# Kernel optimization log

Measured on AMD Instinct MI355X. Metric: run time of the kernel, lower is better.

## Reference

```python
import jax, jax.numpy as jnp
import numpy as np

B, L, D_MODEL = 4, 2048, 1024
D_INNER, D_STATE, D_CONV = 2 * D_MODEL, 16, 4
DT_RANK = (D_MODEL + 15) // 16  # 64


def silu(v):
    return v * jax.nn.sigmoid(v)


def setup_inputs() -> dict:
    key = jax.random.key(0)
    ks = jax.random.split(key, 8)
    n = lambda k, shape, s: jax.random.normal(k, shape, jnp.float32) * s
    A = jnp.broadcast_to(jnp.arange(1, D_STATE + 1, dtype=jnp.float32), (D_INNER, D_STATE))
    return {
        "x": jax.random.normal(ks[0], (B, L, D_MODEL), jnp.float32),
        "in_proj_w": n(ks[1], (2 * D_INNER, D_MODEL), 0.02),
        "conv_w": n(ks[2], (D_INNER, 1, D_CONV), 0.1),
        "conv_b": jnp.zeros((D_INNER,), jnp.float32),
        "x_proj_w": n(ks[3], (DT_RANK + 2 * D_STATE, D_INNER), 0.02),
        "dt_proj_w": n(ks[4], (D_INNER, DT_RANK), 0.1),
        "dt_proj_b": n(ks[5], (D_INNER,), 0.1),
        "A_log": jnp.log(A),
        "D": jnp.ones((D_INNER,), jnp.float32),
        "out_proj_w": n(ks[6], (D_MODEL, D_INNER), 0.02),
        "ln_g": jnp.ones((D_MODEL,), jnp.float32),
        "ln_b": jnp.zeros((D_MODEL,), jnp.float32),
    }


def mamba(x, in_proj_w, conv_w, conv_b, x_proj_w, dt_proj_w, dt_proj_b, A_log, D, out_proj_w):
    # in_proj -> (B, L, 2*d_inner), split into x-branch and gate z
    xz = jnp.einsum("bld,ed->ble", x, in_proj_w)
    xm, z = jnp.split(xz, 2, axis=-1)
    # depthwise causal conv over time
    xc = jnp.swapaxes(xm, 1, 2)  # (B, d_inner, L)
    xc = jax.lax.conv_general_dilated(
        xc, conv_w, (1,), [(D_CONV - 1, 0)],
        dimension_numbers=("NCH", "OIH", "NCH"), feature_group_count=D_INNER,
    ) + conv_b[None, :, None]
    xm = silu(jnp.swapaxes(xc, 1, 2))  # (B, L, d_inner)
    # input-dependent dt, B, C
    dbc = jnp.einsum("bld,ed->ble", xm, x_proj_w)
    dt, Bm, Cm = jnp.split(dbc, [DT_RANK, DT_RANK + D_STATE], axis=-1)
    dt = jax.nn.softplus(jnp.einsum("blr,dr->bld", dt, dt_proj_w) + dt_proj_b)
    A = -jnp.exp(A_log)  # (d_inner, d_state)

    def step(h, inp):
        dt_t, B_t, C_t, x_t = inp  # (B,d_inner),(B,d_state),(B,d_state),(B,d_inner)
        h = jnp.exp(dt_t[..., None] * A) * h + (dt_t * x_t)[..., None] * B_t[:, None, :]
        y = jnp.einsum("bds,bs->bd", h, C_t)
        return h, y

    h0 = jnp.zeros((B, D_INNER, D_STATE), xm.dtype)
    xs = (jnp.swapaxes(dt, 0, 1), jnp.swapaxes(Bm, 0, 1), jnp.swapaxes(Cm, 0, 1), jnp.swapaxes(xm, 0, 1))
    _, ys = jax.lax.scan(step, h0, xs)
    y = jnp.swapaxes(ys, 0, 1) + D * xm  # (B, L, d_inner)
    y = y * silu(z)
    return jnp.einsum("bld,od->blo", y, out_proj_w)


def layer_norm(h, g, b, eps=1e-5):
    mu = jnp.mean(h, axis=-1, keepdims=True)
    var = jnp.mean(jnp.square(h - mu), axis=-1, keepdims=True)
    return (h - mu) * jax.lax.rsqrt(var + eps) * g + b


def reference(x, in_proj_w, conv_w, conv_b, x_proj_w, dt_proj_w, dt_proj_b, A_log, D, out_proj_w, ln_g, ln_b):
    y = mamba(x, in_proj_w, conv_w, conv_b, x_proj_w, dt_proj_w, dt_proj_b, A_log, D, out_proj_w)
    # dropout_level=0 (eval): identity
    return layer_norm(y + x, ln_g, ln_b)
```

## Files before the change

### kernel.cpp

```cpp
#include <hip/hip_runtime.h>
#include <hip/hip_bf16.h>

#define B_ 4
#define L_ 2048
#define DM 1024
#define DI 2048
#define DSTATE 16
#define DTR 64
#define LC 64
#define NC (L_ / LC)
#define LOG2E 1.44269504f

typedef unsigned short ushort_t;
typedef __bf16 bf16x8 __attribute__((ext_vector_type(8)));
typedef float f32x4 __attribute__((ext_vector_type(4)));
typedef float f32x16 __attribute__((ext_vector_type(16)));
typedef unsigned short u16x8 __attribute__((ext_vector_type(8)));
typedef unsigned short u16x4 __attribute__((ext_vector_type(4)));

__device__ __forceinline__ ushort_t f2bf(float f) {
    unsigned u = __builtin_bit_cast(unsigned, f);
    unsigned r = (u + 0x7FFFu + ((u >> 16) & 1u)) >> 16;
    return (ushort_t)r;
}
__device__ __forceinline__ float bf2f(ushort_t h) {
    unsigned u = ((unsigned)h) << 16;
    return __builtin_bit_cast(float, u);
}

#define CV_E0 1048576
#define CV_E1 (CV_E0 + 49152)
#define CV_E2 (CV_E1 + 32768)
#define CV_E3 (CV_E2 + 524288)
#define CV_E4 (CV_E3 + 2097152)
__global__ __launch_bounds__(256) void k_cvt5(
    const float* __restrict__ s0, ushort_t* __restrict__ d0,
    const float* __restrict__ s1, ushort_t* __restrict__ d1,
    const float* __restrict__ s2, ushort_t* __restrict__ d2,
    const float* __restrict__ s3, ushort_t* __restrict__ d3,
    const float* __restrict__ s4, ushort_t* __restrict__ d4) {
    int g = blockIdx.x * 256 + threadIdx.x;
    const float* s;
    ushort_t* dst;
    int i;
    if (g < CV_E0)      { s = s0; dst = d0; i = g * 4; }
    else if (g < CV_E1) { s = s1; dst = d1; i = (g - CV_E0) * 4; }
    else if (g < CV_E2) { s = s2; dst = d2; i = (g - CV_E1) * 4; }
    else if (g < CV_E3) { s = s3; dst = d3; i = (g - CV_E2) * 4; }
    else                { s = s4; dst = d4; i = (g - CV_E3) * 4; }
    float4 v = *reinterpret_cast<const float4*>(s + i);
    ushort4 o;
    o.x = f2bf(v.x); o.y = f2bf(v.y); o.z = f2bf(v.z); o.w = f2bf(v.w);
    *reinterpret_cast<ushort4*>(dst + i) = o;
}

#define FENCE asm volatile("" ::: "memory")
#define VM3 asm volatile("s_waitcnt vmcnt(3)" ::: "memory")
#define VM0 asm volatile("s_waitcnt vmcnt(0)" ::: "memory")

template <int KK, int LDC, int NT>
__global__ __launch_bounds__(512, 2) void k_gemmP(const ushort_t* __restrict__ Aq,
                                                  const ushort_t* __restrict__ Bq,
                                                  ushort_t* __restrict__ C) {
    __shared__ ushort_t lds[36864];
    const int tid = threadIdx.x;
    const int w = tid >> 6, lane = tid & 63;
    const int l15 = lane & 15;
    const int wm = w >> 2, wn = w & 3;
    const int bid = blockIdx.x;
    const int tm = bid & 31, tn = bid >> 5;
    const int row0 = tm * 256, col0 = tn * 128;

    const int rs = w * 16 + (lane >> 2);
    const int lcs = (lane & 3) ^ ((lane >> 3) & 3);
    const int pcr = ((lane >> 4) ^ ((l15 >> 1) & 3)) * 8;
    const int aoff = wm * 4096 + l15 * 32 + pcr;
    const int boff = 8192 + wn * 1024 + l15 * 32 + pcr;

    auto stg = [&](int buf, int t) {
        const ushort_t* sa = Aq + (size_t)(row0 + rs) * KK + t * 32 + lcs * 8;
        __builtin_amdgcn_global_load_lds(
            (const __attribute__((address_space(1))) void*)sa,
            (__attribute__((address_space(3))) void*)&lds[buf * 12288 + w * 512], 16, 0, 0);
        __builtin_amdgcn_global_load_lds(
            (const __attribute__((address_space(1))) void*)(sa + (size_t)128 * KK),
            (__attribute__((address_space(3))) void*)&lds[buf * 12288 + 4096 + w * 512], 16, 0, 0);
        const ushort_t* sb = Bq + (size_t)(col0 + rs) * KK + t * 32 + lcs * 8;
        __builtin_amdgcn_global_load_lds(
            (const __attribute__((address_space(1))) void*)sb,
            (__attribute__((address_space(3))) void*)&lds[buf * 12288 + 8192 + w * 512], 16, 0, 0);
    };

    f32x4 acc[8][2] = {};

#define GPHASE(BUF, STAGE_STMT, WAIT_STMT)                                        \
    {                                                                             \
        bf16x8 av[8], bv[2];                                                      \
        _Pragma("unroll") for (int i_ = 0; i_ < 8; ++i_)                          \
            av[i_] = *(const bf16x8*)&lds[(BUF) * 12288 + aoff + i_ * 512];       \
        _Pragma("unroll") for (int i_ = 0; i_ < 2; ++i_)                          \
            bv[i_] = *(const bf16x8*)&lds[(BUF) * 12288 + boff + i_ * 512];       \
        STAGE_STMT;                                                               \
        FENCE; __builtin_amdgcn_s_barrier(); FENCE;                               \
        asm volatile("s_waitcnt lgkmcnt(0)" ::: "memory");                        \
        __builtin_amdgcn_sched_barrier(0);                                        \
        __builtin_amdgcn_s_setprio(1);                                            \
        _Pragma("unroll") for (int i_ = 0; i_ < 8; ++i_)                          \
            _Pragma("unroll") for (int j_ = 0; j_ < 2; ++j_)                      \
                acc[i_][j_] = __builtin_amdgcn_mfma_f32_16x16x32_bf16(            \
                    av[i_], bv[j_], acc[i_][j_], 0, 0, 0);                        \
        __builtin_amdgcn_s_setprio(0);                                            \
        WAIT_STMT;                                                                \
        FENCE; __builtin_amdgcn_s_barrier(); FENCE;                               \
    }

    stg(0, 0); stg(1, 1);
    VM3;
    FENCE; __builtin_amdgcn_s_barrier(); FENCE;

#pragma unroll 1
    for (int k = 0; k < (NT - 2) / 3; ++k) {
        const int t0 = 3 * k;
        GPHASE(0, stg(2, t0 + 2), VM3);
        GPHASE(1, stg(0, t0 + 3), VM3);
        GPHASE(2, stg(1, t0 + 4), VM3);
    }
    if constexpr ((NT - 2) % 3 == 2) {
        GPHASE(0, stg(2, NT - 2), VM3);
        GPHASE(1, stg(0, NT - 1), VM3);
        GPHASE(2, (void)0, VM0);
        GPHASE(0, (void)0, (void)0);
    } else {
        GPHASE(0, (void)0, VM0);
        GPHASE(1, (void)0, (void)0);
    }
#undef GPHASE

#pragma unroll
    for (int mf = 0; mf < 8; ++mf)
#pragma unroll
        for (int nf = 0; nf < 2; ++nf) {
            int col = col0 + wn * 32 + nf * 16 + l15;
#pragma unroll
            for (int r = 0; r < 4; ++r) {
                int row = row0 + wm * 128 + mf * 16 + (lane >> 4) * 4 + r;
                C[(size_t)row * LDC + col] = f2bf(acc[mf][nf][r]);
            }
        }
}

template <int EPI, bool OUTBF>
__global__ __launch_bounds__(256) void k_gemm2(
    const ushort_t* __restrict__ A, const ushort_t* __restrict__ Bw,
    void* __restrict__ C, const float* __restrict__ bias,
    int M, int N, int K, int lda, int ldb, int ldc, int tilesM) {
    __shared__ ushort_t As[128 * 64];
    __shared__ ushort_t Bs[128 * 64];
    int tid = threadIdx.x;
    int lane = tid & 63, wv = tid >> 6;
    int wr = wv >> 1, wc = wv & 1;
    int bid = blockIdx.x;
    int tilesN = gridDim.x / tilesM;
    int per = 8 * tilesN;
    int grp = bid / per, within = bid % per;
    int tm = grp * 8 + (within & 7);
    int tn = within >> 3;
    int row0 = tm * 128, col0 = tn * 128;
    int kchunk = K / gridDim.z;
    int kbeg = blockIdx.z * kchunk, kend = kbeg + kchunk;
    float* Cf = (float*)C + (size_t)blockIdx.z * (size_t)M * ldc;

    int sr = lane >> 3;
    int sj = lane & 7;
    f32x4 acc[4][4] = {};

    for (int k0 = kbeg; k0 < kend; k0 += 64) {
        __syncthreads();
#pragma unroll
        for (int i = 0; i < 4; ++i) {
            int slot = wv * 4 + i;
            int r = slot * 8 + sr;
            int jA = sj ^ (r & 7);
            __builtin_amdgcn_global_load_lds(
                (const __attribute__((address_space(1))) void*)&A[(size_t)(row0 + r) * lda + k0 + jA * 8],
                (__attribute__((address_space(3))) void*)&As[slot * 512], 16, 0, 0);
            __builtin_amdgcn_global_load_lds(
                (const __attribute__((address_space(1))) void*)&Bw[(size_t)(col0 + r) * ldb + k0 + jA * 8],
                (__attribute__((address_space(3))) void*)&Bs[slot * 512], 16, 0, 0);
        }
        __syncthreads();
#pragma unroll
        for (int kk = 0; kk < 2; ++kk) {
            int co = kk * 32 + (lane >> 4) * 8;
            int sx = (lane & 7) << 3;
            bf16x8 af[4], bfr[4];
#pragma unroll
            for (int m = 0; m < 4; ++m) {
                int rw = wr * 64 + m * 16 + (lane & 15);
                af[m] = *reinterpret_cast<const bf16x8*>(&As[rw * 64 + (co ^ sx)]);
            }
#pragma unroll
            for (int n = 0; n < 4; ++n) {
                int rw = wc * 64 + n * 16 + (lane & 15);
                bfr[n] = *reinterpret_cast<const bf16x8*>(&Bs[rw * 64 + (co ^ sx)]);
            }
#pragma unroll
            for (int m = 0; m < 4; ++m)
#pragma unroll
                for (int n = 0; n < 4; ++n)
                    acc[m][n] = __builtin_amdgcn_mfma_f32_16x16x32_bf16(af[m], bfr[n], acc[m][n], 0, 0, 0);
        }
    }

#pragma unroll
    for (int m = 0; m < 4; ++m) {
#pragma unroll
        for (int n = 0; n < 4; ++n) {
            int col = col0 + wc * 64 + n * 16 + (lane & 15);
            if (col >= N) continue;
#pragma unroll
            for (int r = 0; r < 4; ++r) {
                int row = row0 + wr * 64 + m * 16 + (lane >> 4) * 4 + r;
                float v = acc[m][n][r];
                if (EPI == 1) {
                    v += bias[col];
                    v = (v > 20.f) ? v : log1pf(__expf(v));
                }
                if (OUTBF)
                    ((ushort_t*)C)[(size_t)row * ldc + col] = f2bf(v);
                else
                    Cf[(size_t)row * ldc + col] = v;
            }
        }
    }
}

__global__ __launch_bounds__(256) void k_red4(const float* __restrict__ p,
                                              ushort_t* __restrict__ o,
                                              int n, int stride) {
    int i = (blockIdx.x * 256 + threadIdx.x) * 4;
    if (i >= n) return;
    f32x4 a = *reinterpret_cast<const f32x4*>(&p[i]);
    f32x4 b = *reinterpret_cast<const f32x4*>(&p[i + stride]);
    f32x4 c = *reinterpret_cast<const f32x4*>(&p[i + 2 * stride]);
    f32x4 d = *reinterpret_cast<const f32x4*>(&p[i + 3 * stride]);
    ushort4 r;
    r.x = f2bf(a[0] + b[0] + c[0] + d[0]);
    r.y = f2bf(a[1] + b[1] + c[1] + d[1]);
    r.z = f2bf(a[2] + b[2] + c[2] + d[2]);
    r.w = f2bf(a[3] + b[3] + c[3] + d[3]);
    *reinterpret_cast<ushort4*>(&o[i]) = r;
}

__global__ __launch_bounds__(256) void k_conv(const ushort_t* __restrict__ xz,
                                              const float* __restrict__ w,
                                              const float* __restrict__ bias,
                                              ushort_t* __restrict__ out) {
    int d = blockIdx.x * 256 + threadIdx.x;
    int b = blockIdx.z;
    int t0 = blockIdx.y * 128;
    float w0 = w[d * 4 + 0], w1 = w[d * 4 + 1], w2 = w[d * 4 + 2], w3 = w[d * 4 + 3];
    float bi = bias[d];
    size_t base = ((size_t)b * L_) * (2 * DI) + d;
    size_t obase = ((size_t)b * L_) * DI + d;
    float x0 = (t0 >= 3) ? bf2f(xz[base + (size_t)(t0 - 3) * (2 * DI)]) : 0.f;
    float x1 = (t0 >= 2) ? bf2f(xz[base + (size_t)(t0 - 2) * (2 * DI)]) : 0.f;
    float x2 = (t0 >= 1) ? bf2f(xz[base + (size_t)(t0 - 1) * (2 * DI)]) : 0.f;
    for (int t = t0; t < t0 + 128; ++t) {
        float cur = bf2f(xz[base + (size_t)t * (2 * DI)]);
        float v = w0 * x0 + w1 * x1 + w2 * x2 + w3 * cur + bi;
        v = v / (1.f + __expf(-v));
        out[obase + (size_t)t * DI] = f2bf(v);
        x0 = x1; x1 = x2; x2 = cur;
    }
}

__global__ __launch_bounds__(256) void k_scan1(
    const ushort_t* __restrict__ dt, const ushort_t* __restrict__ xm,
    const ushort_t* __restrict__ dbc, const float* __restrict__ A_log,
    float* __restrict__ hfin, float* __restrict__ dtsum) {
    __shared__ float Bsh[LC][DSTATE];
    int tid = threadIdx.x;
    int d = blockIdx.x * 256 + tid;
    int c = blockIdx.y, b = blockIdx.z;
    f32x16 arow;
    float a1 = __expf(A_log[d * DSTATE]);
    bool ok = true;
#pragma unroll
    for (int s = 0; s < DSTATE; ++s) {
        float av = __expf(A_log[d * DSTATE + s]);
        arow[s] = -av * LOG2E;
        ok = ok && (fabsf(av - (float)(s + 1) * a1) <= 1e-4f * (float)(s + 1) * fabsf(a1) + 1e-6f);
    }
    float arow0 = -a1 * LOG2E;
    size_t rbase = (size_t)b * L_ + (size_t)c * LC;
    {
        int i = tid * 4;
        int t = i >> 4, s0 = i & 15;
        u16x4 v = *reinterpret_cast<const u16x4*>(&dbc[(rbase + t) * 96 + DTR + s0]);
#pragma unroll
        for (int j = 0; j < 4; ++j) Bsh[t][s0 + j] = bf2f(v[j]);
    }
    __syncthreads();
    f32x4 h0 = {}, h1 = {}, h2 = {}, h3 = {};
    float sd = 0.f;
    if (ok) {
        for (int t = 0; t < LC; ++t) {
            size_t ro = rbase + t;
            float dtv = bf2f(dt[ro * DI + d]);
            float xv = bf2f(xm[ro * DI + d]);
            float dx = dtv * xv;
            sd += dtv;
            float p = __builtin_amdgcn_exp2f(dtv * arow0);
            float p2 = p * p, p3 = p2 * p, p4 = p2 * p2;
            f32x4 ea = {p, p2, p3, p4};
            f32x4 eb = ea * p4, ec = eb * p4, ed = ec * p4;
            const f32x4* Bq = reinterpret_cast<const f32x4*>(&Bsh[t][0]);
            h0 = h0 * ea + Bq[0] * dx;
            h1 = h1 * eb + Bq[1] * dx;
            h2 = h2 * ec + Bq[2] * dx;
            h3 = h3 * ed + Bq[3] * dx;
        }
    } else {
        for (int t = 0; t < LC; ++t) {
            size_t ro = rbase + t;
            float dtv = bf2f(dt[ro * DI + d]);
            float xv = bf2f(xm[ro * DI + d]);
            float dx = dtv * xv;
            sd += dtv;
            const f32x4* Bq = reinterpret_cast<const f32x4*>(&Bsh[t][0]);
            f32x4 e0, e1, e2, e3;
#pragma unroll
            for (int j = 0; j < 4; ++j) {
                e0[j] = __builtin_amdgcn_exp2f(dtv * arow[j]);
                e1[j] = __builtin_amdgcn_exp2f(dtv * arow[4 + j]);
                e2[j] = __builtin_amdgcn_exp2f(dtv * arow[8 + j]);
                e3[j] = __builtin_amdgcn_exp2f(dtv * arow[12 + j]);
            }
            h0 = h0 * e0 + Bq[0] * dx;
            h1 = h1 * e1 + Bq[1] * dx;
            h2 = h2 * e2 + Bq[2] * dx;
            h3 = h3 * e3 + Bq[3] * dx;
        }
    }
    size_t hbase = (((size_t)b * NC + c) * DI + d) * DSTATE;
    *reinterpret_cast<f32x4*>(&hfin[hbase + 0]) = h0;
    *reinterpret_cast<f32x4*>(&hfin[hbase + 4]) = h1;
    *reinterpret_cast<f32x4*>(&hfin[hbase + 8]) = h2;
    *reinterpret_cast<f32x4*>(&hfin[hbase + 12]) = h3;
    dtsum[((size_t)b * NC + c) * DI + d] = sd;
}

__global__ __launch_bounds__(256) void k_scan2(
    float* __restrict__ hfin, const float* __restrict__ dtsum,
    const float* __restrict__ A_log) {
    int gid = blockIdx.x * 256 + threadIdx.x;
    int s = gid & (DSTATE - 1);
    int d = (gid >> 4) & (DI - 1);
    int b = gid >> 15;
    float Av = -__expf(A_log[d * DSTATE + s]) * LOG2E;
    float carry = 0.f;
    for (int c = 0; c < NC; ++c) {
        size_t idx = (((size_t)b * NC + c) * DI + d) * DSTATE + s;
        float loc = hfin[idx];
        hfin[idx] = carry;
        float sd = dtsum[((size_t)b * NC + c) * DI + d];
        carry = __builtin_amdgcn_exp2f(Av * sd) * carry + loc;
    }
}

__global__ __launch_bounds__(256) void k_scan3(
    const ushort_t* __restrict__ dt, const ushort_t* __restrict__ xm,
    const ushort_t* __restrict__ xz, const ushort_t* __restrict__ dbc,
    const float* __restrict__ A_log, const float* __restrict__ Dp,
    const float* __restrict__ hinit, ushort_t* __restrict__ yg) {
    __shared__ float Bsh[LC][DSTATE];
    __shared__ float Csh[LC][DSTATE];
    int tid = threadIdx.x;
    int d = blockIdx.x * 256 + tid;
    int c = blockIdx.y, b = blockIdx.z;
    f32x16 arow;
    float a1 = __expf(A_log[d * DSTATE]);
    bool ok = true;
#pragma unroll
    for (int s = 0; s < DSTATE; ++s) {
        float av = __expf(A_log[d * DSTATE + s]);
        arow[s] = -av * LOG2E;
        ok = ok && (fabsf(av - (float)(s + 1) * a1) <= 1e-4f * (float)(s + 1) * fabsf(a1) + 1e-6f);
    }
    float arow0 = -a1 * LOG2E;
    float Dd = Dp[d];
    size_t rbase = (size_t)b * L_ + (size_t)c * LC;
    {
        int e0 = tid * 8;
        int t = e0 >> 5, s0 = e0 & 31;
        u16x8 v = *reinterpret_cast<const u16x8*>(&dbc[(rbase + t) * 96 + DTR + s0]);
#pragma unroll
        for (int j = 0; j < 8; ++j) {
            int s = s0 + j;
            float f = bf2f(v[j]);
            if (s < DSTATE) Bsh[t][s] = f;
            else Csh[t][s - DSTATE] = f;
        }
    }
    __syncthreads();
    size_t hbase = (((size_t)b * NC + c) * DI + d) * DSTATE;
    f32x4 h0 = *reinterpret_cast<const f32x4*>(&hinit[hbase + 0]);
    f32x4 h1 = *reinterpret_cast<const f32x4*>(&hinit[hbase + 4]);
    f32x4 h2 = *reinterpret_cast<const f32x4*>(&hinit[hbase + 8]);
    f32x4 h3 = *reinterpret_cast<const f32x4*>(&hinit[hbase + 12]);
    if (ok) {
        for (int t = 0; t < LC; ++t) {
            size_t ro = rbase + t;
            float dtv = bf2f(dt[ro * DI + d]);
            float xv = bf2f(xm[ro * DI + d]);
            float zv = bf2f(xz[ro * (2 * DI) + DI + d]);
            float dx = dtv * xv;
            float p = __builtin_amdgcn_exp2f(dtv * arow0);
            float p2 = p * p, p3 = p2 * p, p4 = p2 * p2;
            f32x4 ea = {p, p2, p3, p4};
            f32x4 eb = ea * p4, ec = eb * p4, ed = ec * p4;
            const f32x4* Bq = reinterpret_cast<const f32x4*>(&Bsh[t][0]);
            const f32x4* Cq = reinterpret_cast<const f32x4*>(&Csh[t][0]);
            h0 = h0 * ea + Bq[0] * dx;
            h1 = h1 * eb + Bq[1] * dx;
            h2 = h2 * ec + Bq[2] * dx;
            h3 = h3 * ed + Bq[3] * dx;
            f32x4 y4 = h0 * Cq[0] + h1 * Cq[1] + h2 * Cq[2] + h3 * Cq[3];
            float y = (y4[0] + y4[1]) + (y4[2] + y4[3]) + Dd * xv;
            y *= zv / (1.f + __expf(-zv));
            yg[ro * DI + d] = f2bf(y);
        }
    } else {
        for (int t = 0; t < LC; ++t) {
            size_t ro = rbase + t;
            float dtv = bf2f(dt[ro * DI + d]);
            float xv = bf2f(xm[ro * DI + d]);
            float zv = bf2f(xz[ro * (2 * DI) + DI + d]);
            float dx = dtv * xv;
            const f32x4* Bq = reinterpret_cast<const f32x4*>(&Bsh[t][0]);
            const f32x4* Cq = reinterpret_cast<const f32x4*>(&Csh[t][0]);
            f32x4 e0, e1, e2, e3;
#pragma unroll
            for (int j = 0; j < 4; ++j) {
                e0[j] = __builtin_amdgcn_exp2f(dtv * arow[j]);
                e1[j] = __builtin_amdgcn_exp2f(dtv * arow[4 + j]);
                e2[j] = __builtin_amdgcn_exp2f(dtv * arow[8 + j]);
                e3[j] = __builtin_amdgcn_exp2f(dtv * arow[12 + j]);
            }
            h0 = h0 * e0 + Bq[0] * dx;
            h1 = h1 * e1 + Bq[1] * dx;
            h2 = h2 * e2 + Bq[2] * dx;
            h3 = h3 * e3 + Bq[3] * dx;
            f32x4 y4 = h0 * Cq[0] + h1 * Cq[1] + h2 * Cq[2] + h3 * Cq[3];
            float y = (y4[0] + y4[1]) + (y4[2] + y4[3]) + Dd * xv;
            y *= zv / (1.f + __expf(-zv));
            yg[ro * DI + d] = f2bf(y);
        }
    }
}

__global__ __launch_bounds__(256) void k_ln(const ushort_t* __restrict__ mo,
                                            const float* __restrict__ x,
                                            const float* __restrict__ g,
                                            const float* __restrict__ be,
                                            float* __restrict__ out) {
    __shared__ float red[8];
    size_t r = blockIdx.x;
    int tid = threadIdx.x;
    ushort4 mv = *reinterpret_cast<const ushort4*>(&mo[r * DM + tid * 4]);
    float4 xv = *reinterpret_cast<const float4*>(&x[r * DM + tid * 4]);
    float h0 = bf2f(mv.x) + xv.x, h1 = bf2f(mv.y) + xv.y;
    float h2 = bf2f(mv.z) + xv.z, h3 = bf2f(mv.w) + xv.w;
    float s = h0 + h1 + h2 + h3;
    float q = h0 * h0 + h1 * h1 + h2 * h2 + h3 * h3;
#pragma unroll
    for (int o = 32; o > 0; o >>= 1) {
        s += __shfl_down(s, o);
        q += __shfl_down(q, o);
    }
    int lane = tid & 63, wid = tid >> 6;
    if (lane == 0) { red[wid] = s; red[4 + wid] = q; }
    __syncthreads();
    s = red[0] + red[1] + red[2] + red[3];
    q = red[4] + red[5] + red[6] + red[7];
    float mu = s * (1.f / DM);
    float var = q * (1.f / DM) - mu * mu;
    float rs = rsqrtf(var + 1e-5f);
    float4 gv = *reinterpret_cast<const float4*>(&g[tid * 4]);
    float4 bv = *reinterpret_cast<const float4*>(&be[tid * 4]);
    float4 o;
    o.x = (h0 - mu) * rs * gv.x + bv.x;
    o.y = (h1 - mu) * rs * gv.y + bv.y;
    o.z = (h2 - mu) * rs * gv.z + bv.z;
    o.w = (h3 - mu) * rs * gv.w + bv.w;
    *reinterpret_cast<float4*>(&out[r * DM + tid * 4]) = o;
}

extern "C" void kernel_launch(void* const* d_in, const int* in_sizes, int n_in,
                              void* d_out, int out_size, void* d_ws, size_t ws_size,
                              hipStream_t stream) {
    const float* x      = (const float*)d_in[0];
    const float* w_in   = (const float*)d_in[1];
    const float* conv_w = (const float*)d_in[2];
    const float* conv_b = (const float*)d_in[3];
    const float* w_xp   = (const float*)d_in[4];
    const float* w_dt   = (const float*)d_in[5];
    const float* dt_b   = (const float*)d_in[6];
    const float* A_log  = (const float*)d_in[7];
    const float* Dp     = (const float*)d_in[8];
    const float* w_out  = (const float*)d_in[9];
    const float* ln_g   = (const float*)d_in[10];
    const float* ln_b   = (const float*)d_in[11];
    float* out = (float*)d_out;

    char* ws = (char*)d_ws;
    size_t off = 0;
    auto alloc = [&](size_t bytes) -> void* {
        void* p = ws + off;
        off += (bytes + 255) & ~(size_t)255;
        return p;
    };
    const int M = B_ * L_;
    ushort_t* w_in_b  = (ushort_t*)alloc((size_t)2 * DI * DM * 2);
    ushort_t* w_xp_b  = (ushort_t*)alloc((size_t)96 * DI * 2);
    ushort_t* w_dt_b  = (ushort_t*)alloc((size_t)DI * DTR * 2);
    ushort_t* w_out_b = (ushort_t*)alloc((size_t)DM * DI * 2);
    ushort_t* x_b     = (ushort_t*)alloc((size_t)M * DM * 2);
    ushort_t* xz      = (ushort_t*)alloc((size_t)M * 2 * DI * 2);
    ushort_t* xm      = (ushort_t*)alloc((size_t)M * DI * 2);
    ushort_t* dbc     = (ushort_t*)alloc((size_t)M * 96 * 2);
    ushort_t* dtb     = (ushort_t*)alloc((size_t)M * DI * 2);
    ushort_t* yg      = (ushort_t*)alloc((size_t)M * DI * 2);
    float*    dtsum   = (float*)alloc((size_t)B_ * NC * DI * 4);
    float*    dbc_p   = (float*)alloc((size_t)4 * M * 96 * 4);
    ushort_t* mo      = dtb;
    float*    hfin    = (float*)x_b;

    k_cvt5<<<dim3(CV_E4 / 256), 256, 0, stream>>>(
        w_in, w_in_b, w_xp, w_xp_b, w_dt, w_dt_b, w_out, w_out_b, x, x_b);

    k_gemmP<1024, 4096, 32><<<dim3(1024), 512, 0, stream>>>(x_b, w_in_b, xz);
    k_conv<<<dim3(DI / 256, L_ / 128, B_), 256, 0, stream>>>(xz, conv_w, conv_b, xm);
    k_gemm2<0, false><<<dim3(64, 1, 4), 256, 0, stream>>>(
        xm, w_xp_b, dbc_p, nullptr, M, 96, DI, DI, DI, 96, 64);
    k_red4<<<dim3((M * 96 / 4 + 255) / 256), 256, 0, stream>>>(dbc_p, dbc, M * 96, M * 96);
    k_gemm2<1, true><<<dim3(64 * 16, 1, 1), 256, 0, stream>>>(
        dbc, w_dt_b, dtb, dt_b, M, DI, DTR, 96, DTR, DI, 64);
    k_scan1<<<dim3(DI / 256, NC, B_), 256, 0, stream>>>(dtb, xm, dbc, A_log, hfin, dtsum);
    k_scan2<<<dim3(B_ * DI * DSTATE / 256), 256, 0, stream>>>(hfin, dtsum, A_log);
    k_scan3<<<dim3(DI / 256, NC, B_), 256, 0, stream>>>(dtb, xm, xz, dbc, A_log, Dp, hfin, yg);
    k_gemmP<2048, 1024, 64><<<dim3(256), 512, 0, stream>>>(yg, w_out_b, mo);
    k_ln<<<dim3(M), 256, 0, stream>>>(mo, x, ln_g, ln_b, out);
}
```

Before: 330.0 us.

## Split in_proj GEMM into two launches and use smaller-tile out_proj GEMM

Adds a 128x128-tile GEMM kernel (k_gemmQ) with 256 threads, triple-buffered LDS staging and occupancy hint 3, and uses it for the out_proj GEMM. The old path launched only 256 blocks of 256x128 tiles there, so the GPU was under-filled; 512 blocks give more parallelism. The in_proj GEMM is split into two half-width launches (x-branch and z-branch columns), which adds a launch and may reduce overlap in exchange for smaller waves.

```diff
diff --git a/kernel.cpp b/kernel.cpp
--- a/kernel.cpp
+++ b/kernel.cpp
@@ -55,6 +55,7 @@
 }
 
 #define FENCE asm volatile("" ::: "memory")
+#define VM4 asm volatile("s_waitcnt vmcnt(4)" ::: "memory")
 #define VM3 asm volatile("s_waitcnt vmcnt(3)" ::: "memory")
 #define VM0 asm volatile("s_waitcnt vmcnt(0)" ::: "memory")
 
@@ -144,6 +145,100 @@
 #pragma unroll
             for (int r = 0; r < 4; ++r) {
                 int row = row0 + wm * 128 + mf * 16 + (lane >> 4) * 4 + r;
+                C[(size_t)row * LDC + col] = f2bf(acc[mf][nf][r]);
+            }
+        }
+}
+
+template <int KK, int LDC, int NT, int TM>
+__global__ __launch_bounds__(256, 3) void k_gemmQ(const ushort_t* __restrict__ Aq,
+                                                  const ushort_t* __restrict__ Bq,
+                                                  ushort_t* __restrict__ C) {
+    __shared__ ushort_t lds[24576];
+    const int tid = threadIdx.x;
+    const int w = tid >> 6, lane = tid & 63;
+    const int l15 = lane & 15;
+    const int wm = w >> 1, wn = w & 1;
+    const int bid = blockIdx.x;
+    const int tm = bid & (TM - 1), tn = bid / TM;
+    const int row0 = tm * 128, col0 = tn * 128;
+
+    const int rs = w * 16 + (lane >> 2);
+    const int lcs = (lane & 3) ^ ((lane >> 3) & 3);
+    const int pcr = ((lane >> 4) ^ ((l15 >> 1) & 3)) * 8;
+    const int aoff = wm * 2048 + l15 * 32 + pcr;
+    const int boff = 4096 + wn * 2048 + l15 * 32 + pcr;
+
+    auto stg = [&](int buf, int t) {
+        const ushort_t* sa = Aq + (size_t)(row0 + rs) * KK + t * 32 + lcs * 8;
+        __builtin_amdgcn_global_load_lds(
+            (const __attribute__((address_space(1))) void*)sa,
+            (__attribute__((address_space(3))) void*)&lds[buf * 8192 + w * 512], 16, 0, 0);
+        __builtin_amdgcn_global_load_lds(
+            (const __attribute__((address_space(1))) void*)(sa + (size_t)64 * KK),
+            (__attribute__((address_space(3))) void*)&lds[buf * 8192 + 2048 + w * 512], 16, 0, 0);
+        const ushort_t* sb = Bq + (size_t)(col0 + rs) * KK + t * 32 + lcs * 8;
+        __builtin_amdgcn_global_load_lds(
+            (const __attribute__((address_space(1))) void*)sb,
+            (__attribute__((address_space(3))) void*)&lds[buf * 8192 + 4096 + w * 512], 16, 0, 0);
+        __builtin_amdgcn_global_load_lds(
+            (const __attribute__((address_space(1))) void*)(sb + (size_t)64 * KK),
+            (__attribute__((address_space(3))) void*)&lds[buf * 8192 + 6144 + w * 512], 16, 0, 0);
+    };
+
+    f32x4 acc[4][4] = {};
+
+#define QPHASE(BUF, STAGE_STMT, WAIT_STMT)                                        \
+    {                                                                             \
+        bf16x8 av[4], bv[4];                                                      \
+        _Pragma("unroll") for (int i_ = 0; i_ < 4; ++i_)                          \
+            av[i_] = *(const bf16x8*)&lds[(BUF) * 8192 + aoff + i_ * 512];        \
+        _Pragma("unroll") for (int i_ = 0; i_ < 4; ++i_)                          \
+            bv[i_] = *(const bf16x8*)&lds[(BUF) * 8192 + boff + i_ * 512];        \
+        STAGE_STMT;                                                               \
+        FENCE; __builtin_amdgcn_s_barrier(); FENCE;                               \
+        asm volatile("s_waitcnt lgkmcnt(0)" ::: "memory");                        \
+        __builtin_amdgcn_sched_barrier(0);                                        \
+        __builtin_amdgcn_s_setprio(1);                                            \
+        _Pragma("unroll") for (int i_ = 0; i_ < 4; ++i_)                          \
+            _Pragma("unroll") for (int j_ = 0; j_ < 4; ++j_)                      \
+                acc[i_][j_] = __builtin_amdgcn_mfma_f32_16x16x32_bf16(            \
+                    av[i_], bv[j_], acc[i_][j_], 0, 0, 0);                        \
+        __builtin_amdgcn_s_setprio(0);                                            \
+        WAIT_STMT;                                                                \
+        FENCE; __builtin_amdgcn_s_barrier(); FENCE;                               \
+    }
+
+    stg(0, 0); stg(1, 1);
+    VM4;
+    FENCE; __builtin_amdgcn_s_barrier(); FENCE;
+
+#pragma unroll 1
+    for (int k = 0; k < (NT - 2) / 3; ++k) {
+        const int t0 = 3 * k;
+        QPHASE(0, stg(2, t0 + 2), VM4);
+        QPHASE(1, stg(0, t0 + 3), VM4);
+        QPHASE(2, stg(1, t0 + 4), VM4);
+    }
+    if constexpr ((NT - 2) % 3 == 2) {
+        QPHASE(0, stg(2, NT - 2), VM4);
+        QPHASE(1, stg(0, NT - 1), VM4);
+        QPHASE(2, (void)0, VM0);
+        QPHASE(0, (void)0, (void)0);
+    } else {
+        QPHASE(0, (void)0, VM0);
+        QPHASE(1, (void)0, (void)0);
+    }
+#undef QPHASE
+
+#pragma unroll
+    for (int mf = 0; mf < 4; ++mf)
+#pragma unroll
+        for (int nf = 0; nf < 4; ++nf) {
+            int col = col0 + wn * 64 + nf * 16 + l15;
+#pragma unroll
+            for (int r = 0; r < 4; ++r) {
+                int row = row0 + wm * 64 + mf * 16 + (lane >> 4) * 4 + r;
                 C[(size_t)row * LDC + col] = f2bf(acc[mf][nf][r]);
             }
         }
@@ -540,7 +635,9 @@
     k_cvt5<<<dim3(CV_E4 / 256), 256, 0, stream>>>(
         w_in, w_in_b, w_xp, w_xp_b, w_dt, w_dt_b, w_out, w_out_b, x, x_b);
 
-    k_gemmP<1024, 4096, 32><<<dim3(1024), 512, 0, stream>>>(x_b, w_in_b, xz);
+    k_gemmP<1024, 4096, 32><<<dim3(512), 512, 0, stream>>>(x_b, w_in_b, xz);
+    k_gemmP<1024, 4096, 32><<<dim3(512), 512, 0, stream>>>(
+        x_b, w_in_b + (size_t)2048 * 1024, xz + 2048);
     k_conv<<<dim3(DI / 256, L_ / 128, B_), 256, 0, stream>>>(xz, conv_w, conv_b, xm);
     k_gemm2<0, false><<<dim3(64, 1, 4), 256, 0, stream>>>(
         xm, w_xp_b, dbc_p, nullptr, M, 96, DI, DI, DI, 96, 64);
@@ -550,6 +647,6 @@
     k_scan1<<<dim3(DI / 256, NC, B_), 256, 0, stream>>>(dtb, xm, dbc, A_log, hfin, dtsum);
     k_scan2<<<dim3(B_ * DI * DSTATE / 256), 256, 0, stream>>>(hfin, dtsum, A_log);
     k_scan3<<<dim3(DI / 256, NC, B_), 256, 0, stream>>>(dtb, xm, xz, dbc, A_log, Dp, hfin, yg);
-    k_gemmP<2048, 1024, 64><<<dim3(256), 512, 0, stream>>>(yg, w_out_b, mo);
+    k_gemmQ<2048, 1024, 64, 64><<<dim3(512), 256, 0, stream>>>(yg, w_out_b, mo);
     k_ln<<<dim3(M), 256, 0, stream>>>(mo, x, ln_g, ln_b, out);
 }
```

New measurement: 334.3 us. About the same (+1.3%).
